# Optimization experiments

Measured on AMD Instinct MI355X. Metric: run time of the kernel, lower is better.

The kernel has to match this reference:

```python
import jax, jax.numpy as jnp
import numpy as np

B, K, D_IN, H, DH, OBS = 8192, 64, 256, 8, 32, 32
REP = H * DH  # 256
EPS = 1e-6
LN_EPS = 1e-5


def setup_inputs() -> dict:
    key = jax.random.key(0)
    ks = jax.random.split(key, 12)
    s = lambda i, shape, sc=0.02: (jax.random.normal(ks[i], shape, jnp.float32) * sc)
    return {
        "x_anchor": jax.random.normal(ks[0], (B, D_IN), jnp.float32),
        "x_neighbors": jax.random.normal(ks[1], (B, K, D_IN), jnp.float32),
        "edge_weights": jax.random.uniform(ks[2], (B, K), jnp.float32),
        "g_local": jax.random.normal(ks[3], (B, OBS), jnp.float32),
        # anchor_proj: Linear(input_dim, rep_dim) + LayerNorm(rep_dim)
        "W_anchor": s(4, (REP, D_IN)), "b_anchor": jnp.zeros((REP,), jnp.float32),
        "g_anchor": jnp.ones((REP,), jnp.float32), "beta_anchor": jnp.zeros((REP,), jnp.float32),
        # nei_proj
        "W_nei": s(5, (REP, D_IN)), "b_nei": jnp.zeros((REP,), jnp.float32),
        "g_nei": jnp.ones((REP,), jnp.float32), "beta_nei": jnp.zeros((REP,), jnp.float32),
        "view_embed": s(6, (DH,), 0.01),
        # per-head q/k/v/out linears stacked as [H, out, in]
        "Wq": s(7, (H, DH, DH)), "Wk": s(8, (H, DH, DH)),
        "Wv": s(9, (H, DH, DH)), "Wo": s(10, (H, DH, DH)),
        # geom_scale_net: Linear(obs_dim, n_heads)
        "W_geom": s(11, (H, OBS)), "b_geom": jnp.zeros((H,), jnp.float32),
    }


def _ln(x, g, b):
    m = jnp.mean(x, axis=-1, keepdims=True)
    v = jnp.mean((x - m) ** 2, axis=-1, keepdims=True)
    return (x - m) * jax.lax.rsqrt(v + LN_EPS) * g + b


def reference(x_anchor, x_neighbors, edge_weights, g_local,
              W_anchor, b_anchor, g_anchor, beta_anchor,
              W_nei, b_nei, g_nei, beta_nei,
              view_embed, Wq, Wk, Wv, Wo, W_geom, b_geom):
    # anchor projection + view-embed token: [B, H, DH]
    h_anchor = _ln(x_anchor @ W_anchor.T + b_anchor, g_anchor, beta_anchor)
    h_anchor = h_anchor.reshape(B, H, DH) + view_embed  # broadcast [DH]
    # neighbor projection: [B, K, H, DH]
    h_nei = _ln(x_neighbors @ W_nei.T + b_nei, g_nei, beta_nei).reshape(B, K, H, DH)
    # per-head linears as one batched contraction (W is [H, out, in])
    q = jnp.einsum('bhd,hod->bho', h_anchor, Wq)          # [B, H, DH]
    k = jnp.einsum('bkhd,hod->bkho', h_nei, Wk)           # [B, K, H, DH]
    v = jnp.einsum('bkhd,hod->bkho', h_nei, Wv)           # [B, K, H, DH]
    scores = jnp.einsum('bhd,bkhd->bhk', q, k) / np.float32(np.sqrt(DH))
    # adaptive per-row, per-head tau (softplus) applied to log edge weights
    geom_scale = jax.nn.softplus(g_local @ W_geom.T + b_geom)[:, :, None]  # [B, H, 1]
    scores = scores + geom_scale * jnp.log(edge_weights[:, None, :] + EPS)
    attn = jax.nn.softmax(scores, axis=-1)  # dropout is identity in eval
    head_out = jnp.einsum('bhk,bkhd->bhd', attn, v)       # [B, H, DH]
    head_out = jnp.einsum('bhd,hod->bho', head_out, Wo) + h_anchor
    return head_out, attn
```

## Files before the change

kernel.cpp:

```cpp
#include <hip/hip_runtime.h>
#include <hip/hip_bf16.h>

typedef __bf16 bf16x8 __attribute__((ext_vector_type(8)));
typedef float  f32x4  __attribute__((ext_vector_type(4)));
typedef unsigned short u16;
typedef u16 u16x8 __attribute__((ext_vector_type(8)));

__device__ __forceinline__ u16 f2bf(float f) {
    unsigned u = __float_as_uint(f);
    u += 0x7FFFu + ((u >> 16) & 1u);
    return (u16)(u >> 16);
}
__device__ __forceinline__ float bf2f(u16 s) {
    return __uint_as_float(((unsigned)s) << 16);
}

__device__ __forceinline__ void stage_tile(const float* __restrict__ src, char* buf, int t) {
#pragma unroll
    for (int i = 0; i < 8; ++i) {
        int flat = i * 2048 + t * 8;
        float4 a = *(const float4*)(src + flat);
        float4 b = *(const float4*)(src + flat + 4);
        int row  = flat >> 8;
        int colb = (flat & 255) * 2;
        u16x8 v;
        v[0]=f2bf(a.x); v[1]=f2bf(a.y); v[2]=f2bf(a.z); v[3]=f2bf(a.w);
        v[4]=f2bf(b.x); v[5]=f2bf(b.y); v[6]=f2bf(b.z); v[7]=f2bf(b.w);
        *(u16x8*)(buf + row*512 + (colb ^ ((row & 7) << 4))) = v;
    }
}

__device__ __forceinline__ void gemm_tile(const char* buf, const u16* __restrict__ WB,
                                          int w, int l, f32x4 acc[4][4]) {
#pragma unroll
    for (int mt = 0; mt < 4; mt++)
#pragma unroll
        for (int nt = 0; nt < 4; nt++) acc[mt][nt] = (f32x4){0.f,0.f,0.f,0.f};
#pragma unroll
    for (int ks = 0; ks < 8; ks++) {
        bf16x8 bfrag[4];
#pragma unroll
        for (int nt = 0; nt < 4; nt++)
            bfrag[nt] = *(const bf16x8*)(WB + (((ks*16) + (w*4 + nt))*64 + l)*8);
        bf16x8 afrag[4];
#pragma unroll
        for (int mt = 0; mt < 4; mt++) {
            int row  = mt*16 + (l & 15);
            int colb = ks*64 + ((l >> 4) << 4);
            afrag[mt] = *(const bf16x8*)(buf + row*512 + (colb ^ ((row & 7) << 4)));
        }
#pragma unroll
        for (int mt = 0; mt < 4; mt++)
#pragma unroll
            for (int nt = 0; nt < 4; nt++)
                acc[mt][nt] = __builtin_amdgcn_mfma_f32_16x16x32_bf16(
                    afrag[mt], bfrag[nt], acc[mt][nt], 0, 0, 0);
    }
}

__global__ void k_prep(const float* __restrict__ Wa, const float* __restrict__ Wn,
                       const float* __restrict__ Wq, const float* __restrict__ Wk,
                       u16* __restrict__ WaB, u16* __restrict__ WnB,
                       u16* __restrict__ WqF, u16* __restrict__ WkF) {
    int i = blockIdx.x * 256 + threadIdx.x;
    int j = i & 7, l = (i >> 3) & 63, ntg = (i >> 9) & 15, ks = i >> 13;
    int n = ntg*16 + (l & 15), k = ks*32 + ((l >> 4) << 3) + j;
    WaB[i] = f2bf(Wa[n*256 + k]);
    WnB[i] = f2bf(Wn[n*256 + k]);
    if (i < 8192) {
        int nt = (i >> 9) & 1, h = i >> 10;
        int n2 = nt*16 + (l & 15), e = ((l >> 4) << 3) + j;
        WqF[i] = f2bf(Wq[h*1024 + n2*32 + e]);
        WkF[i] = f2bf(Wk[h*1024 + n2*32 + e]);
    }
}

__global__ __launch_bounds__(256, 3) void k_anchor(
    const float* __restrict__ xa, const float* __restrict__ gl,
    const float* __restrict__ b_anc, const float* __restrict__ g_anc,
    const float* __restrict__ be_anc, const float* __restrict__ ve,
    const float* __restrict__ Wgeom, const float* __restrict__ bgeom,
    const u16* __restrict__ WaB, const u16* __restrict__ WqF,
    float* __restrict__ ha, float* __restrict__ qws, float* __restrict__ gsws) {
    __shared__ __align__(16) char smem[32768 + 2048];
    const int t = threadIdx.x, w = t >> 6, l = t & 63;
    const int b0 = blockIdx.x * 64;

    stage_tile(xa + (size_t)b0 * 256, smem, t);
    __syncthreads();

    f32x4 acc[4][4];
    gemm_tile(smem, WaB, w, l, acc);

    float bn[4];
#pragma unroll
    for (int nt = 0; nt < 4; nt++) bn[nt] = b_anc[w*64 + nt*16 + (l & 15)];
#pragma unroll
    for (int mt = 0; mt < 4; mt++)
#pragma unroll
        for (int nt = 0; nt < 4; nt++)
#pragma unroll
            for (int r = 0; r < 4; r++) acc[mt][nt][r] += bn[nt];

    float2* PART = (float2*)(smem + 32768);
#pragma unroll
    for (int mt = 0; mt < 4; mt++)
#pragma unroll
        for (int r = 0; r < 4; r++) {
            float s  = acc[mt][0][r] + acc[mt][1][r] + acc[mt][2][r] + acc[mt][3][r];
            float qq = acc[mt][0][r]*acc[mt][0][r] + acc[mt][1][r]*acc[mt][1][r]
                     + acc[mt][2][r]*acc[mt][2][r] + acc[mt][3][r]*acc[mt][3][r];
#pragma unroll
            for (int m2 = 1; m2 < 16; m2 <<= 1) { s += __shfl_xor(s, m2); qq += __shfl_xor(qq, m2); }
            if ((l & 15) == 0) PART[w*64 + mt*16 + ((l >> 4) << 2) + r] = make_float2(s, qq);
        }
    __syncthreads();

    float gg[4], bb2[4], vv[4];
#pragma unroll
    for (int nt = 0; nt < 4; nt++) {
        int col = w*64 + nt*16 + (l & 15);
        gg[nt] = g_anc[col]; bb2[nt] = be_anc[col];
        vv[nt] = ve[((nt & 1) << 4) + (l & 15)];
    }
#pragma unroll
    for (int mt = 0; mt < 4; mt++)
#pragma unroll
        for (int r = 0; r < 4; r++) {
            int row = mt*16 + ((l >> 4) << 2) + r;
            float2 p0 = PART[row], p1 = PART[64+row], p2 = PART[128+row], p3 = PART[192+row];
            float mean = (p0.x+p1.x+p2.x+p3.x) * (1.f/256.f);
            float var  = (p0.y+p1.y+p2.y+p3.y) * (1.f/256.f) - mean*mean;
            float rs   = rsqrtf(var + 1e-5f);
#pragma unroll
            for (int nt = 0; nt < 4; nt++) {
                int col = w*64 + nt*16 + (l & 15);
                float x = (acc[mt][nt][r] - mean)*rs*gg[nt] + bb2[nt] + vv[nt];
                ha[(size_t)(b0+row)*256 + col] = x;
                *(u16*)(smem + row*512 + ((col*2) ^ ((row & 7) << 4))) = f2bf(x);
            }
        }
    __syncthreads();

#pragma unroll
    for (int hh = 0; hh < 2; hh++) {
        int h = 2*w + hh;
        bf16x8 af[4];
#pragma unroll
        for (int mt = 0; mt < 4; mt++) {
            int row = mt*16 + (l & 15);
            int colb = h*64 + ((l >> 4) << 4);
            af[mt] = *(const bf16x8*)(smem + row*512 + (colb ^ ((row & 7) << 4)));
        }
        bf16x8 bf0 = *(const bf16x8*)(WqF + ((h*2 + 0)*64 + l)*8);
        bf16x8 bf1 = *(const bf16x8*)(WqF + ((h*2 + 1)*64 + l)*8);
        f32x4 qa[4][2];
#pragma unroll
        for (int mt = 0; mt < 4; mt++) {
            qa[mt][0] = (f32x4){0.f,0.f,0.f,0.f};
            qa[mt][1] = (f32x4){0.f,0.f,0.f,0.f};
            qa[mt][0] = __builtin_amdgcn_mfma_f32_16x16x32_bf16(af[mt], bf0, qa[mt][0], 0,0,0);
            qa[mt][1] = __builtin_amdgcn_mfma_f32_16x16x32_bf16(af[mt], bf1, qa[mt][1], 0,0,0);
        }
#pragma unroll
        for (int mt = 0; mt < 4; mt++)
#pragma unroll
            for (int nt = 0; nt < 2; nt++)
#pragma unroll
                for (int r = 0; r < 4; r++) {
                    int row = mt*16 + ((l >> 4) << 2) + r;
                    int d = nt*16 + (l & 15);
                    qws[(size_t)(b0+row)*256 + h*32 + d] = qa[mt][nt][r] * 0.17677669529663687f;
                }
    }

    for (int task = t; task < 512; task += 256) {
        int row = task >> 3, h = task & 7;
        const float* g = gl + (size_t)(b0+row)*32;
        float x = bgeom[h];
#pragma unroll
        for (int e = 0; e < 32; e++) x += g[e] * Wgeom[h*32 + e];
        gsws[(size_t)(b0+row)*8 + h] = (x > 20.f) ? x : log1pf(__expf(x));
    }
}

#define SM_AT 32768
#define SM_Z  (32768+2048)
#define SM_PO (32768+3072)
#define SM_EL (32768+4096)
__global__ __launch_bounds__(256, 3) void k_main(
    const float* __restrict__ xn, const float* __restrict__ ew,
    const float* __restrict__ b_nei, const float* __restrict__ g_nei,
    const float* __restrict__ be_nei,
    const float* __restrict__ Wv, const float* __restrict__ Wo,
    const u16* __restrict__ WnB, const u16* __restrict__ WkF,
    const float* __restrict__ ha, const float* __restrict__ qws,
    const float* __restrict__ gsws, float* __restrict__ outp, int Btot) {
    __shared__ __align__(16) char smem[37120];
    const int t = threadIdx.x, w = t >> 6, l = t & 63;
    const int b = blockIdx.x;

    stage_tile(xn + (size_t)b * 16384, smem, t);
    if (t < 64) ((float*)(smem + SM_EL))[t] = __logf(ew[(size_t)b*64 + t] + 1e-6f);
    __syncthreads();

    f32x4 acc[4][4];
    gemm_tile(smem, WnB, w, l, acc);

    float bn[4];
#pragma unroll
    for (int nt = 0; nt < 4; nt++) bn[nt] = b_nei[w*64 + nt*16 + (l & 15)];
#pragma unroll
    for (int mt = 0; mt < 4; mt++)
#pragma unroll
        for (int nt = 0; nt < 4; nt++)
#pragma unroll
            for (int r = 0; r < 4; r++) acc[mt][nt][r] += bn[nt];

    float2* PART = (float2*)(smem + SM_AT);
#pragma unroll
    for (int mt = 0; mt < 4; mt++)
#pragma unroll
        for (int r = 0; r < 4; r++) {
            float s  = acc[mt][0][r] + acc[mt][1][r] + acc[mt][2][r] + acc[mt][3][r];
            float qq = acc[mt][0][r]*acc[mt][0][r] + acc[mt][1][r]*acc[mt][1][r]
                     + acc[mt][2][r]*acc[mt][2][r] + acc[mt][3][r]*acc[mt][3][r];
#pragma unroll
            for (int m2 = 1; m2 < 16; m2 <<= 1) { s += __shfl_xor(s, m2); qq += __shfl_xor(qq, m2); }
            if ((l & 15) == 0) PART[w*64 + mt*16 + ((l >> 4) << 2) + r] = make_float2(s, qq);
        }
    __syncthreads();

    float gg[4], bb2[4];
#pragma unroll
    for (int nt = 0; nt < 4; nt++) {
        int col = w*64 + nt*16 + (l & 15);
        gg[nt] = g_nei[col]; bb2[nt] = be_nei[col];
    }
#pragma unroll
    for (int mt = 0; mt < 4; mt++)
#pragma unroll
        for (int r = 0; r < 4; r++) {
            int row = mt*16 + ((l >> 4) << 2) + r;
            float2 p0 = PART[row], p1 = PART[64+row], p2 = PART[128+row], p3 = PART[192+row];
            float mean = (p0.x+p1.x+p2.x+p3.x) * (1.f/256.f);
            float var  = (p0.y+p1.y+p2.y+p3.y) * (1.f/256.f) - mean*mean;
            float rs   = rsqrtf(var + 1e-5f);
#pragma unroll
            for (int nt = 0; nt < 4; nt++) {
                int col = w*64 + nt*16 + (l & 15);
                float x = (acc[mt][nt][r] - mean)*rs*gg[nt] + bb2[nt];
                *(u16*)(smem + row*512 + ((col*2) ^ ((row & 7) << 4))) = f2bf(x);
            }
        }
    __syncthreads();

    const float* EL = (const float*)(smem + SM_EL);
    float* AT = (float*)(smem + SM_AT);
#pragma unroll
    for (int hh = 0; hh < 2; hh++) {
        int h = 2*w + hh;
        bf16x8 af[4];
#pragma unroll
        for (int mt = 0; mt < 4; mt++) {
            int row = mt*16 + (l & 15);
            int colb = h*64 + ((l >> 4) << 4);
            af[mt] = *(const bf16x8*)(smem + row*512 + (colb ^ ((row & 7) << 4)));
        }
        bf16x8 bf0 = *(const bf16x8*)(WkF + ((h*2 + 0)*64 + l)*8);
        bf16x8 bf1 = *(const bf16x8*)(WkF + ((h*2 + 1)*64 + l)*8);
        f32x4 ka0[4], ka1[4];
#pragma unroll
        for (int mt = 0; mt < 4; mt++) {
            ka0[mt] = (f32x4){0.f,0.f,0.f,0.f};
            ka1[mt] = (f32x4){0.f,0.f,0.f,0.f};
            ka0[mt] = __builtin_amdgcn_mfma_f32_16x16x32_bf16(af[mt], bf0, ka0[mt], 0,0,0);
            ka1[mt] = __builtin_amdgcn_mfma_f32_16x16x32_bf16(af[mt], bf1, ka1[mt], 0,0,0);
        }
        float qv0 = qws[(size_t)b*256 + h*32 + (l & 15)];
        float qv1 = qws[(size_t)b*256 + h*32 + 16 + (l & 15)];
        float gsv = gsws[(size_t)b*8 + h];
        float ps[4][4];
#pragma unroll
        for (int mt = 0; mt < 4; mt++)
#pragma unroll
            for (int r = 0; r < 4; r++) {
                float s = ka0[mt][r]*qv0 + ka1[mt][r]*qv1;
#pragma unroll
                for (int m2 = 1; m2 < 16; m2 <<= 1) s += __shfl_xor(s, m2);
                ps[mt][r] = s + gsv * EL[mt*16 + ((l >> 4) << 2) + r];
            }
        float mx = -1e30f;
#pragma unroll
        for (int mt = 0; mt < 4; mt++)
#pragma unroll
            for (int r = 0; r < 4; r++) mx = fmaxf(mx, ps[mt][r]);
        mx = fmaxf(mx, __shfl_xor(mx, 16));
        mx = fmaxf(mx, __shfl_xor(mx, 32));
        float ex[4][4]; float sm = 0.f;
#pragma unroll
        for (int mt = 0; mt < 4; mt++)
#pragma unroll
            for (int r = 0; r < 4; r++) { ex[mt][r] = __expf(ps[mt][r] - mx); sm += ex[mt][r]; }
        sm += __shfl_xor(sm, 16);
        sm += __shfl_xor(sm, 32);
        float inv = 1.f / sm;
        if ((l & 15) == 0) {
#pragma unroll
            for (int mt = 0; mt < 4; mt++) {
                float4 v4 = make_float4(ex[mt][0]*inv, ex[mt][1]*inv, ex[mt][2]*inv, ex[mt][3]*inv);
                *(float4*)(AT + h*64 + mt*16 + ((l >> 4) << 2)) = v4;
            }
        }
    }
    __syncthreads();

    const size_t ATT_OFF = (size_t)Btot * 256;
#pragma unroll
    for (int i = t; i < 512; i += 256) outp[ATT_OFF + (size_t)b*512 + i] = AT[i];

    int h = t >> 5, e2 = t & 31;
    float z = 0.f;
#pragma unroll
    for (int k = 0; k < 64; k++) {
        float a = AT[h*64 + k];
        u16 hv = *(const u16*)(smem + k*512 + (((h*64) + (e2 << 1)) ^ ((k & 7) << 4)));
        z += a * bf2f(hv);
    }
    ((float*)(smem + SM_Z))[t] = z;
    __syncthreads();

    float po = 0.f;
    {
        const float* wv = Wv + h*1024 + (t & 31)*32;
        const float* zz = (const float*)(smem + SM_Z) + h*32;
#pragma unroll
        for (int e = 0; e < 32; e++) po += wv[e] * zz[e];
    }
    ((float*)(smem + SM_PO))[t] = po;
    __syncthreads();

    float o = 0.f;
    {
        const float* wo = Wo + h*1024 + (t & 31)*32;
        const float* pp = (const float*)(smem + SM_PO) + h*32;
#pragma unroll
        for (int d = 0; d < 32; d++) o += wo[d] * pp[d];
    }
    o += ha[(size_t)b*256 + t];
    outp[(size_t)b*256 + t] = o;
}

extern "C" void kernel_launch(void* const* d_in, const int* in_sizes, int n_in,
                              void* d_out, int out_size, void* d_ws, size_t ws_size,
                              hipStream_t stream) {
    const float* xa  = (const float*)d_in[0];
    const float* xn  = (const float*)d_in[1];
    const float* ew  = (const float*)d_in[2];
    const float* gl  = (const float*)d_in[3];
    const float* Wa  = (const float*)d_in[4];
    const float* ba  = (const float*)d_in[5];
    const float* ga  = (const float*)d_in[6];
    const float* bea = (const float*)d_in[7];
    const float* Wn  = (const float*)d_in[8];
    const float* bn  = (const float*)d_in[9];
    const float* gn  = (const float*)d_in[10];
    const float* ben = (const float*)d_in[11];
    const float* ve  = (const float*)d_in[12];
    const float* Wq  = (const float*)d_in[13];
    const float* Wk  = (const float*)d_in[14];
    const float* Wv  = (const float*)d_in[15];
    const float* Wo  = (const float*)d_in[16];
    const float* Wg  = (const float*)d_in[17];
    const float* bg  = (const float*)d_in[18];
    int B = in_sizes[0] / 256;

    char* ws = (char*)d_ws;
    u16* WnB  = (u16*)(ws + 0);
    u16* WaB  = (u16*)(ws + 131072);
    u16* WqF  = (u16*)(ws + 262144);
    u16* WkF  = (u16*)(ws + 278528);
    float* ha   = (float*)(ws + 294912);
    float* qws  = (float*)(ws + 294912 + 8388608);
    float* gsws = (float*)(ws + 294912 + 16777216);
    float* outp = (float*)d_out;

    hipLaunchKernelGGL(k_prep, dim3(256), dim3(256), 0, stream,
                       Wa, Wn, Wq, Wk, WaB, WnB, WqF, WkF);
    hipLaunchKernelGGL(k_anchor, dim3(B/64), dim3(256), 0, stream,
                       xa, gl, ba, ga, bea, ve, Wg, bg, WaB, WqF, ha, qws, gsws);
    hipLaunchKernelGGL(k_main, dim3(B), dim3(256), 0, stream,
                       xn, ew, bn, gn, ben, Wv, Wo, WnB, WkF, ha, qws, gsws, outp, B);
}
```

Before: 923.1 us.

## Fold Wk into query and Wo into Wv, process four rows per block with prefetch

Precomputes Wk^T·Wq (scaled) and Wo·Wv per head in a new prep kernel. Scores can then be computed as the query-folded vector dotted with the neighbor features, and the output as one fused matrix applied to the attention-weighted sum. This removes the per-row K-projection MFMAs and one of the two small matvecs. k_main now processes four batch rows per block and prefetches the next row's neighbor tile into registers while the current row computes. Staging uses packed bf16 converts. The cost is higher register pressure and fewer blocks in the grid, plus changed rounding from folding the weights before bf16 quantization.

Measured after the change: 1.274 ms. +38.0%, slower.

```diff
diff --git a/kernel.cpp b/kernel.cpp
--- a/kernel.cpp
+++ b/kernel.cpp
@@ -59,19 +59,45 @@
 }
 
 __global__ void k_prep(const float* __restrict__ Wa, const float* __restrict__ Wn,
-                       const float* __restrict__ Wq, const float* __restrict__ Wk,
-                       u16* __restrict__ WaB, u16* __restrict__ WnB,
-                       u16* __restrict__ WqF, u16* __restrict__ WkF) {
+                       u16* __restrict__ WaB, u16* __restrict__ WnB) {
     int i = blockIdx.x * 256 + threadIdx.x;
     int j = i & 7, l = (i >> 3) & 63, ntg = (i >> 9) & 15, ks = i >> 13;
     int n = ntg*16 + (l & 15), k = ks*32 + ((l >> 4) << 3) + j;
     WaB[i] = f2bf(Wa[n*256 + k]);
     WnB[i] = f2bf(Wn[n*256 + k]);
-    if (i < 8192) {
-        int nt = (i >> 9) & 1, h = i >> 10;
+}
+
+__global__ void k_prep2(const float* __restrict__ Wq, const float* __restrict__ Wk,
+                        const float* __restrict__ Wv, const float* __restrict__ Wo,
+                        u16* __restrict__ WqkF, float* __restrict__ Wvo) {
+    __shared__ float sWq[1024], sWk[1024], sWv[1024], sWo[1024], sQK[1024];
+    const int h = blockIdx.x, t = threadIdx.x;
+#pragma unroll
+    for (int i = 0; i < 4; i++) {
+        int idx = i*256 + t;
+        sWq[idx] = Wq[h*1024 + idx]; sWk[idx] = Wk[h*1024 + idx];
+        sWv[idx] = Wv[h*1024 + idx]; sWo[idx] = Wo[h*1024 + idx];
+    }
+    __syncthreads();
+#pragma unroll
+    for (int i = 0; i < 4; i++) {
+        int idx = i*256 + t, f = idx >> 5, e = idx & 31;
+        float a1 = 0.f, a2 = 0.f;
+#pragma unroll
+        for (int d = 0; d < 32; d++) {
+            a1 += sWk[d*32 + f] * sWq[d*32 + e];
+            a2 += sWo[f*32 + d] * sWv[d*32 + e];
+        }
+        sQK[f*32 + e] = a1 * 0.17677669529663687f;
+        Wvo[h*1024 + idx] = a2;
+    }
+    __syncthreads();
+#pragma unroll
+    for (int i = 0; i < 4; i++) {
+        int idx2 = i*256 + t;
+        int j = idx2 & 7, l = (idx2 >> 3) & 63, nt = idx2 >> 9;
         int n2 = nt*16 + (l & 15), e = ((l >> 4) << 3) + j;
-        WqF[i] = f2bf(Wq[h*1024 + n2*32 + e]);
-        WkF[i] = f2bf(Wk[h*1024 + n2*32 + e]);
+        WqkF[h*1024 + idx2] = f2bf(sQK[n2*32 + e]);
     }
 }
 
@@ -80,8 +106,8 @@
     const float* __restrict__ b_anc, const float* __restrict__ g_anc,
     const float* __restrict__ be_anc, const float* __restrict__ ve,
     const float* __restrict__ Wgeom, const float* __restrict__ bgeom,
-    const u16* __restrict__ WaB, const u16* __restrict__ WqF,
-    float* __restrict__ ha, float* __restrict__ qws, float* __restrict__ gsws) {
+    const u16* __restrict__ WaB, const u16* __restrict__ WqkF,
+    float* __restrict__ ha, float* __restrict__ qkws, float* __restrict__ gsws) {
     __shared__ __align__(16) char smem[32768 + 2048];
     const int t = threadIdx.x, w = t >> 6, l = t & 63;
     const int b0 = blockIdx.x * 64;
@@ -152,8 +178,8 @@
             int colb = h*64 + ((l >> 4) << 4);
             af[mt] = *(const bf16x8*)(smem + row*512 + (colb ^ ((row & 7) << 4)));
         }
-        bf16x8 bf0 = *(const bf16x8*)(WqF + ((h*2 + 0)*64 + l)*8);
-        bf16x8 bf1 = *(const bf16x8*)(WqF + ((h*2 + 1)*64 + l)*8);
+        bf16x8 bf0 = *(const bf16x8*)(WqkF + ((h*2 + 0)*64 + l)*8);
+        bf16x8 bf1 = *(const bf16x8*)(WqkF + ((h*2 + 1)*64 + l)*8);
         f32x4 qa[4][2];
 #pragma unroll
         for (int mt = 0; mt < 4; mt++) {
@@ -170,7 +196,7 @@
                 for (int r = 0; r < 4; r++) {
                     int row = mt*16 + ((l >> 4) << 2) + r;
                     int d = nt*16 + (l & 15);
-                    qws[(size_t)(b0+row)*256 + h*32 + d] = qa[mt][nt][r] * 0.17677669529663687f;
+                    qkws[(size_t)(b0+row)*256 + h*32 + d] = qa[mt][nt][r];
                 }
     }
 
@@ -184,171 +210,192 @@
     }
 }
 
-#define SM_AT 32768
-#define SM_Z  (32768+2048)
-#define SM_PO (32768+3072)
-#define SM_EL (32768+4096)
+#define ROWS 4
 __global__ __launch_bounds__(256, 3) void k_main(
     const float* __restrict__ xn, const float* __restrict__ ew,
     const float* __restrict__ b_nei, const float* __restrict__ g_nei,
     const float* __restrict__ be_nei,
-    const float* __restrict__ Wv, const float* __restrict__ Wo,
-    const u16* __restrict__ WnB, const u16* __restrict__ WkF,
-    const float* __restrict__ ha, const float* __restrict__ qws,
+    const float* __restrict__ Wvo, const u16* __restrict__ WnB,
+    const float* __restrict__ ha, const float* __restrict__ qkws,
     const float* __restrict__ gsws, float* __restrict__ outp, int Btot) {
-    __shared__ __align__(16) char smem[37120];
+    __shared__ __align__(16) char smem[32768 + 2048 + 1024 + 1024];
+    float* PART_AT = (float*)(smem + 32768);
+    float* ZBUF    = (float*)(smem + 32768+2048);
+    float* QKB     = (float*)(smem + 32768+3072);
     const int t = threadIdx.x, w = t >> 6, l = t & 63;
-    const int b = blockIdx.x;
-
-    stage_tile(xn + (size_t)b * 16384, smem, t);
-    if (t < 64) ((float*)(smem + SM_EL))[t] = __logf(ew[(size_t)b*64 + t] + 1e-6f);
-    __syncthreads();
-
-    f32x4 acc[4][4];
-    gemm_tile(smem, WnB, w, l, acc);
-
-    float bn[4];
-#pragma unroll
-    for (int nt = 0; nt < 4; nt++) bn[nt] = b_nei[w*64 + nt*16 + (l & 15)];
-#pragma unroll
-    for (int mt = 0; mt < 4; mt++)
-#pragma unroll
-        for (int nt = 0; nt < 4; nt++)
-#pragma unroll
-            for (int r = 0; r < 4; r++) acc[mt][nt][r] += bn[nt];
-
-    float2* PART = (float2*)(smem + SM_AT);
-#pragma unroll
-    for (int mt = 0; mt < 4; mt++)
-#pragma unroll
-        for (int r = 0; r < 4; r++) {
-            float s  = acc[mt][0][r] + acc[mt][1][r] + acc[mt][2][r] + acc[mt][3][r];
-            float qq = acc[mt][0][r]*acc[mt][0][r] + acc[mt][1][r]*acc[mt][1][r]
-                     + acc[mt][2][r]*acc[mt][2][r] + acc[mt][3][r]*acc[mt][3][r];
-#pragma unroll
-            for (int m2 = 1; m2 < 16; m2 <<= 1) { s += __shfl_xor(s, m2); qq += __shfl_xor(qq, m2); }
-            if ((l & 15) == 0) PART[w*64 + mt*16 + ((l >> 4) << 2) + r] = make_float2(s, qq);
-        }
-    __syncthreads();
-
-    float gg[4], bb2[4];
-#pragma unroll
-    for (int nt = 0; nt < 4; nt++) {
-        int col = w*64 + nt*16 + (l & 15);
-        gg[nt] = g_nei[col]; bb2[nt] = be_nei[col];
-    }
-#pragma unroll
-    for (int mt = 0; mt < 4; mt++)
-#pragma unroll
-        for (int r = 0; r < 4; r++) {
-            int row = mt*16 + ((l >> 4) << 2) + r;
-            float2 p0 = PART[row], p1 = PART[64+row], p2 = PART[128+row], p3 = PART[192+row];
-            float mean = (p0.x+p1.x+p2.x+p3.x) * (1.f/256.f);
-            float var  = (p0.y+p1.y+p2.y+p3.y) * (1.f/256.f) - mean*mean;
-            float rs   = rsqrtf(var + 1e-5f);
-#pragma unroll
-            for (int nt = 0; nt < 4; nt++) {
-                int col = w*64 + nt*16 + (l & 15);
-                float x = (acc[mt][nt][r] - mean)*rs*gg[nt] + bb2[nt];
-                *(u16*)(smem + row*512 + ((col*2) ^ ((row & 7) << 4))) = f2bf(x);
-            }
-        }
-    __syncthreads();
-
-    const float* EL = (const float*)(smem + SM_EL);
-    float* AT = (float*)(smem + SM_AT);
-#pragma unroll
-    for (int hh = 0; hh < 2; hh++) {
-        int h = 2*w + hh;
-        bf16x8 af[4];
-#pragma unroll
-        for (int mt = 0; mt < 4; mt++) {
-            int row = mt*16 + (l & 15);
-            int colb = h*64 + ((l >> 4) << 4);
-            af[mt] = *(const bf16x8*)(smem + row*512 + (colb ^ ((row & 7) << 4)));
-        }
-        bf16x8 bf0 = *(const bf16x8*)(WkF + ((h*2 + 0)*64 + l)*8);
-        bf16x8 bf1 = *(const bf16x8*)(WkF + ((h*2 + 1)*64 + l)*8);
-        f32x4 ka0[4], ka1[4];
-#pragma unroll
-        for (int mt = 0; mt < 4; mt++) {
-            ka0[mt] = (f32x4){0.f,0.f,0.f,0.f};
-            ka1[mt] = (f32x4){0.f,0.f,0.f,0.f};
-            ka0[mt] = __builtin_amdgcn_mfma_f32_16x16x32_bf16(af[mt], bf0, ka0[mt], 0,0,0);
-            ka1[mt] = __builtin_amdgcn_mfma_f32_16x16x32_bf16(af[mt], bf1, ka1[mt], 0,0,0);
-        }
-        float qv0 = qws[(size_t)b*256 + h*32 + (l & 15)];
-        float qv1 = qws[(size_t)b*256 + h*32 + 16 + (l & 15)];
-        float gsv = gsws[(size_t)b*8 + h];
-        float ps[4][4];
+    const int b0 = blockIdx.x * ROWS;
+    const float4* src4 = (const float4*)xn;
+    const size_t ATT_OFF = (size_t)Btot * 256;
+
+    float4 st[16]; float4 qkp;
+    {
+        size_t B4 = (size_t)b0 * 4096;
+#pragma unroll
+        for (int i = 0; i < 8; i++) {
+            st[2*i]   = src4[B4 + i*512 + t*2];
+            st[2*i+1] = src4[B4 + i*512 + t*2 + 1];
+        }
+        if (t < 64) qkp = ((const float4*)qkws)[(size_t)b0*64 + t];
+    }
+
+#pragma unroll
+    for (int r = 0; r < ROWS; r++) {
+        const int b = b0 + r;
+#pragma unroll
+        for (int i = 0; i < 8; i++) {
+            int flat = i*2048 + t*8;
+            int row = flat >> 8, colb = (flat & 255) * 2;
+            float4 a = st[2*i], c = st[2*i+1];
+            unsigned p0, p1, p2, p3;
+            asm("v_cvt_pk_bf16_f32 %0,%1,%2" : "=v"(p0) : "v"(a.x), "v"(a.y));
+            asm("v_cvt_pk_bf16_f32 %0,%1,%2" : "=v"(p1) : "v"(a.z), "v"(a.w));
+            asm("v_cvt_pk_bf16_f32 %0,%1,%2" : "=v"(p2) : "v"(c.x), "v"(c.y));
+            asm("v_cvt_pk_bf16_f32 %0,%1,%2" : "=v"(p3) : "v"(c.z), "v"(c.w));
+            *(uint4*)(smem + row*512 + (colb ^ ((row & 7) << 4))) = make_uint4(p0, p1, p2, p3);
+        }
+        if (t < 64) ((float4*)QKB)[t] = qkp;
+        __syncthreads();
+
+        if (r + 1 < ROWS) {
+            size_t B4 = (size_t)(b+1) * 4096;
+#pragma unroll
+            for (int i = 0; i < 4; i++) {
+                st[2*i]   = src4[B4 + i*512 + t*2];
+                st[2*i+1] = src4[B4 + i*512 + t*2 + 1];
+            }
+            if (t < 64) qkp = ((const float4*)qkws)[(size_t)(b+1)*64 + t];
+        }
+
+        f32x4 acc[4][4];
+        gemm_tile(smem, WnB, w, l, acc);
+        float bn[4];
+#pragma unroll
+        for (int nt = 0; nt < 4; nt++) bn[nt] = b_nei[w*64 + nt*16 + (l & 15)];
 #pragma unroll
         for (int mt = 0; mt < 4; mt++)
 #pragma unroll
-            for (int r = 0; r < 4; r++) {
-                float s = ka0[mt][r]*qv0 + ka1[mt][r]*qv1;
-#pragma unroll
-                for (int m2 = 1; m2 < 16; m2 <<= 1) s += __shfl_xor(s, m2);
-                ps[mt][r] = s + gsv * EL[mt*16 + ((l >> 4) << 2) + r];
-            }
-        float mx = -1e30f;
+            for (int nt = 0; nt < 4; nt++)
+#pragma unroll
+                for (int rr = 0; rr < 4; rr++) acc[mt][nt][rr] += bn[nt];
+
+        float2* PART = (float2*)PART_AT;
 #pragma unroll
         for (int mt = 0; mt < 4; mt++)
 #pragma unroll
-            for (int r = 0; r < 4; r++) mx = fmaxf(mx, ps[mt][r]);
-        mx = fmaxf(mx, __shfl_xor(mx, 16));
-        mx = fmaxf(mx, __shfl_xor(mx, 32));
-        float ex[4][4]; float sm = 0.f;
+            for (int rr = 0; rr < 4; rr++) {
+                float s  = acc[mt][0][rr] + acc[mt][1][rr] + acc[mt][2][rr] + acc[mt][3][rr];
+                float qq = acc[mt][0][rr]*acc[mt][0][rr] + acc[mt][1][rr]*acc[mt][1][rr]
+                         + acc[mt][2][rr]*acc[mt][2][rr] + acc[mt][3][rr]*acc[mt][3][rr];
+#pragma unroll
+                for (int m2 = 1; m2 < 16; m2 <<= 1) { s += __shfl_xor(s, m2); qq += __shfl_xor(qq, m2); }
+                if ((l & 15) == 0) PART[w*64 + mt*16 + ((l >> 4) << 2) + rr] = make_float2(s, qq);
+            }
+        __syncthreads();
+
+        float gg[4], bb2[4];
+#pragma unroll
+        for (int nt = 0; nt < 4; nt++) {
+            int col = w*64 + nt*16 + (l & 15);
+            gg[nt] = g_nei[col]; bb2[nt] = be_nei[col];
+        }
 #pragma unroll
         for (int mt = 0; mt < 4; mt++)
 #pragma unroll
-            for (int r = 0; r < 4; r++) { ex[mt][r] = __expf(ps[mt][r] - mx); sm += ex[mt][r]; }
-        sm += __shfl_xor(sm, 16);
-        sm += __shfl_xor(sm, 32);
-        float inv = 1.f / sm;
-        if ((l & 15) == 0) {
-#pragma unroll
-            for (int mt = 0; mt < 4; mt++) {
-                float4 v4 = make_float4(ex[mt][0]*inv, ex[mt][1]*inv, ex[mt][2]*inv, ex[mt][3]*inv);
-                *(float4*)(AT + h*64 + mt*16 + ((l >> 4) << 2)) = v4;
-            }
-        }
-    }
-    __syncthreads();
-
-    const size_t ATT_OFF = (size_t)Btot * 256;
-#pragma unroll
-    for (int i = t; i < 512; i += 256) outp[ATT_OFF + (size_t)b*512 + i] = AT[i];
-
-    int h = t >> 5, e2 = t & 31;
-    float z = 0.f;
-#pragma unroll
-    for (int k = 0; k < 64; k++) {
-        float a = AT[h*64 + k];
-        u16 hv = *(const u16*)(smem + k*512 + (((h*64) + (e2 << 1)) ^ ((k & 7) << 4)));
-        z += a * bf2f(hv);
-    }
-    ((float*)(smem + SM_Z))[t] = z;
-    __syncthreads();
-
-    float po = 0.f;
-    {
-        const float* wv = Wv + h*1024 + (t & 31)*32;
-        const float* zz = (const float*)(smem + SM_Z) + h*32;
-#pragma unroll
-        for (int e = 0; e < 32; e++) po += wv[e] * zz[e];
-    }
-    ((float*)(smem + SM_PO))[t] = po;
-    __syncthreads();
-
-    float o = 0.f;
-    {
-        const float* wo = Wo + h*1024 + (t & 31)*32;
-        const float* pp = (const float*)(smem + SM_PO) + h*32;
-#pragma unroll
-        for (int d = 0; d < 32; d++) o += wo[d] * pp[d];
-    }
-    o += ha[(size_t)b*256 + t];
-    outp[(size_t)b*256 + t] = o;
+            for (int rr = 0; rr < 4; rr++) {
+                int row = mt*16 + ((l >> 4) << 2) + rr;
+                float2 p0 = PART[row], p1 = PART[64+row], p2 = PART[128+row], p3 = PART[192+row];
+                float mean = (p0.x+p1.x+p2.x+p3.x) * (1.f/256.f);
+                float var  = (p0.y+p1.y+p2.y+p3.y) * (1.f/256.f) - mean*mean;
+                float rs   = rsqrtf(var + 1e-5f);
+#pragma unroll
+                for (int nt = 0; nt < 4; nt++) {
+                    int col = w*64 + nt*16 + (l & 15);
+                    float x = (acc[mt][nt][rr] - mean)*rs*gg[nt] + bb2[nt];
+                    *(u16*)(smem + row*512 + ((col*2) ^ ((row & 7) << 4))) = f2bf(x);
+                }
+            }
+
+        if (r + 1 < ROWS) {
+            size_t B4 = (size_t)(b+1) * 4096;
+#pragma unroll
+            for (int i = 4; i < 8; i++) {
+                st[2*i]   = src4[B4 + i*512 + t*2];
+                st[2*i+1] = src4[B4 + i*512 + t*2 + 1];
+            }
+        }
+        __syncthreads();
+
+        {
+            const int h = t >> 5, k0 = t & 31;
+            const float gsv = gsws[(size_t)b*8 + h];
+            float4 q4[8];
+#pragma unroll
+            for (int j = 0; j < 8; j++) q4[j] = ((const float4*)QKB)[h*8 + j];
+            float s0 = 0.f, s1 = 0.f;
+            const int swz = (k0 & 7) << 4;
+#pragma unroll
+            for (int j = 0; j < 4; j++) {
+                int colb = h*64 + j*16;
+                u16x8 r0 = *(const u16x8*)(smem + k0*512       + (colb ^ swz));
+                u16x8 r1 = *(const u16x8*)(smem + (k0+32)*512  + (colb ^ swz));
+#pragma unroll
+                for (int e = 0; e < 8; e++) {
+                    float qv = ((const float*)q4)[j*8 + e];
+                    s0 += bf2f(r0[e]) * qv;
+                    s1 += bf2f(r1[e]) * qv;
+                }
+            }
+            s0 += gsv * __logf(ew[(size_t)b*64 + k0] + 1e-6f);
+            s1 += gsv * __logf(ew[(size_t)b*64 + k0 + 32] + 1e-6f);
+            float mx = fmaxf(s0, s1);
+#pragma unroll
+            for (int m2 = 1; m2 < 32; m2 <<= 1) mx = fmaxf(mx, __shfl_xor(mx, m2));
+            float e0 = __expf(s0 - mx), e1 = __expf(s1 - mx);
+            float sm = e0 + e1;
+#pragma unroll
+            for (int m2 = 1; m2 < 32; m2 <<= 1) sm += __shfl_xor(sm, m2);
+            float inv = 1.f / sm;
+            e0 *= inv; e1 *= inv;
+            PART_AT[h*64 + k0]      = e0;
+            PART_AT[h*64 + k0 + 32] = e1;
+            size_t ao = ATT_OFF + (size_t)b*512 + h*64;
+            outp[ao + k0]      = e0;
+            outp[ao + k0 + 32] = e1;
+        }
+        __syncthreads();
+
+        {
+            float z = 0.f;
+            const float4* AT4 = (const float4*)PART_AT;
+            const int hh = t >> 5;
+#pragma unroll
+            for (int kk = 0; kk < 16; kk++) {
+                float4 a4 = AT4[hh*16 + kk];
+#pragma unroll
+                for (int q = 0; q < 4; q++) {
+                    int k = kk*4 + q;
+                    u16 hv = *(const u16*)(smem + k*512 + ((2*t) ^ ((k & 7) << 4)));
+                    z += ((const float*)&a4)[q] * bf2f(hv);
+                }
+            }
+            ZBUF[t] = z;
+        }
+        __syncthreads();
+
+        {
+            const int h = t >> 5, oi = t & 31;
+            const float4* wv4 = (const float4*)(Wvo + (h*32 + oi)*32);
+            const float* zz = ZBUF + h*32;
+            float o = 0.f;
+#pragma unroll
+            for (int e4 = 0; e4 < 8; e4++) {
+                float4 wv = wv4[e4];
+                o += wv.x*zz[e4*4] + wv.y*zz[e4*4+1] + wv.z*zz[e4*4+2] + wv.w*zz[e4*4+3];
+            }
+            o += ha[(size_t)b*256 + t];
+            outp[(size_t)b*256 + t] = o;
+        }
+    }
 }
 
 extern "C" void kernel_launch(void* const* d_in, const int* in_sizes, int n_in,
@@ -376,19 +423,19 @@
     int B = in_sizes[0] / 256;
 
     char* ws = (char*)d_ws;
-    u16* WnB  = (u16*)(ws + 0);
-    u16* WaB  = (u16*)(ws + 131072);
-    u16* WqF  = (u16*)(ws + 262144);
-    u16* WkF  = (u16*)(ws + 278528);
-    float* ha   = (float*)(ws + 294912);
-    float* qws  = (float*)(ws + 294912 + 8388608);
-    float* gsws = (float*)(ws + 294912 + 16777216);
+    u16*   WnB  = (u16*)(ws + 0);
+    u16*   WaB  = (u16*)(ws + 131072);
+    u16*   WqkF = (u16*)(ws + 262144);
+    float* Wvo  = (float*)(ws + 278528);
+    float* haP  = (float*)(ws + 311296);
+    float* qkws = (float*)(ws + 311296 + 8388608);
+    float* gsws = (float*)(ws + 311296 + 16777216);
     float* outp = (float*)d_out;
 
-    hipLaunchKernelGGL(k_prep, dim3(256), dim3(256), 0, stream,
-                       Wa, Wn, Wq, Wk, WaB, WnB, WqF, WkF);
+    hipLaunchKernelGGL(k_prep, dim3(256), dim3(256), 0, stream, Wa, Wn, WaB, WnB);
+    hipLaunchKernelGGL(k_prep2, dim3(8), dim3(256), 0, stream, Wq, Wk, Wv, Wo, WqkF, Wvo);
     hipLaunchKernelGGL(k_anchor, dim3(B/64), dim3(256), 0, stream,
-                       xa, gl, ba, ga, bea, ve, Wg, bg, WaB, WqF, ha, qws, gsws);
-    hipLaunchKernelGGL(k_main, dim3(B), dim3(256), 0, stream,
-                       xn, ew, bn, gn, ben, Wv, Wo, WnB, WkF, ha, qws, gsws, outp, B);
-}
+                       xa, gl, ba, ga, bea, ve, Wg, bg, WaB, WqkF, haP, qkws, gsws);
+    hipLaunchKernelGGL(k_main, dim3(B/ROWS), dim3(256), 0, stream,
+                       xn, ew, bn, gn, ben, Wvo, WnB, haP, qkws, gsws, outp, B);
+}
```
